# Kernel optimization log

Hardware: AMD Instinct MI355X
Metric: run time of the kernel (lower is better)

The kernel has to match this reference:

```python
import jax, jax.numpy as jnp
import numpy as np

EPS = 1e-5

def binary_activation(x):
    # ReActNet piecewise-polynomial STE: forward = sign(x), grad follows poly
    m1 = (x < -1).astype(x.dtype)
    m2 = (x < 0).astype(x.dtype)
    m3 = (x < 1).astype(x.dtype)
    out1 = -1.0 * m1 + (x * x + 2.0 * x) * (1.0 - m1)
    out2 = out1 * m2 + (-x * x + 2.0 * x) * (1.0 - m2)
    out3 = out2 * m3 + 1.0 * (1.0 - m3)
    return jax.lax.stop_gradient(jnp.sign(x) - out3) + out3

def binary_conv(x, w, stride, padding):
    # per-output-channel scaled sign weights with clamp STE
    scale = jnp.mean(jnp.abs(w), axis=(1, 2, 3), keepdims=True)
    clipped = jnp.clip(w, -1.0, 1.0)
    bw = jax.lax.stop_gradient(scale * jnp.sign(w) - clipped) + clipped
    return jax.lax.conv_general_dilated(
        x, bw, window_strides=(stride, stride),
        padding=[(padding, padding), (padding, padding)],
        dimension_numbers=('NCHW', 'OIHW', 'NCHW'))

def batch_norm(x, g, b):
    mu = jnp.mean(x, axis=(0, 2, 3), keepdims=True)
    var = jnp.mean((x - mu) ** 2, axis=(0, 2, 3), keepdims=True)
    xn = (x - mu) * jax.lax.rsqrt(var + EPS)
    return xn * g[None, :, None, None] + b[None, :, None, None]

def prelu(x, a):
    a = a[None, :, None, None]
    return jnp.where(x >= 0, x, a * x)

def setup_inputs() -> dict:
    key = jax.random.key(0)
    ks = jax.random.split(key, 12)
    N, C, H, W = 32, 256, 56, 56
    d = {
        'x': jax.random.normal(ks[0], (N, C, H, W), jnp.float32),
        'b11': jax.random.normal(ks[1], (1, C, 1, 1), jnp.float32) * 0.1,
        'b12': jax.random.normal(ks[2], (1, C, 1, 1), jnp.float32) * 0.1,
        'b13': jax.random.normal(ks[3], (1, C, 1, 1), jnp.float32) * 0.1,
        'b21': jax.random.normal(ks[4], (1, C, 1, 1), jnp.float32) * 0.1,
        'b22': jax.random.normal(ks[5], (1, C, 1, 1), jnp.float32) * 0.1,
        'b23': jax.random.normal(ks[6], (1, C, 1, 1), jnp.float32) * 0.1,
        'w3x3': jax.random.normal(ks[7], (C, C, 3, 3), jnp.float32) * 0.05,
        'wpw': jax.random.normal(ks[8], (C, C, 1, 1), jnp.float32) * 0.05,
        'g1': jnp.ones((C,), jnp.float32),
        'be1': jnp.zeros((C,), jnp.float32),
        'g2': jnp.ones((C,), jnp.float32),
        'be2': jnp.zeros((C,), jnp.float32),
        'p1': jnp.full((C,), 0.25, jnp.float32),
        'p2': jnp.full((C,), 0.25, jnp.float32),
    }
    return d

def reference(x, b11, b12, b13, b21, b22, b23, w3x3, wpw, g1, be1, g2, be2, p1, p2):
    # stride=1, inplanes == planes branch
    out1 = binary_activation(x + b11)
    out1 = binary_conv(out1, w3x3, stride=1, padding=1)
    out1 = batch_norm(out1, g1, be1)
    out1 = x + out1
    out1 = prelu(out1 + b12, p1) + b13
    out2 = binary_activation(out1 + b21)
    out2 = binary_conv(out2, wpw, stride=1, padding=0)
    out2 = batch_norm(out2, g2, be2)
    out2 = out2 + out1
    out2 = prelu(out2 + b22, p2) + b23
    return out2
```

## Files before the change

### kernel.cpp

```cpp
#include <hip/hip_runtime.h>

typedef __attribute__((ext_vector_type(4))) float  f32x4;
typedef __attribute__((ext_vector_type(4))) short  s16x4;
typedef __attribute__((ext_vector_type(4))) int    i32x4;

#define MFMAI8(a, b, c) __builtin_amdgcn_mfma_i32_16x16x64_i8((a), (b), (c), 0, 0, 0)

__device__ __forceinline__ void gload_lds16(const void* g, void* l) {
  __builtin_amdgcn_global_load_lds((const __attribute__((address_space(1))) void*)g,
                                   (__attribute__((address_space(3))) void*)l, 16, 0, 0);
}

__device__ __forceinline__ char sgn8(float v) {
  return v > 0.f ? (char)1 : (v < 0.f ? (char)-1 : (char)0);
}

__global__ __launch_bounds__(256) void prep_w(const float* __restrict__ w3,
                                              const float* __restrict__ wpw,
                                              char* __restrict__ w1s,
                                              char* __restrict__ w2s,
                                              float* __restrict__ scale1,
                                              float* __restrict__ scale2) {
  const int o = blockIdx.x;
  const int t = threadIdx.x;
  float s = 0.f;
  if (blockIdx.y == 0) {
    for (int u = t; u < 2304; u += 256) {
      int i = u / 9, tap = u % 9;
      float v = w3[(size_t)(o * 256 + i) * 9 + tap];
      s += fabsf(v);
      w1s[(size_t)(tap * 256 + o) * 256 + i] = sgn8(v);
    }
  } else {
    float v = wpw[o * 256 + t];
    s = fabsf(v);
    w2s[o * 256 + t] = sgn8(v);
  }
  for (int m = 1; m < 64; m <<= 1) s += __shfl_xor(s, m);
  __shared__ float red[4];
  if ((t & 63) == 0) red[t >> 6] = s;
  __syncthreads();
  if (t == 0) {
    float tot = red[0] + red[1] + red[2] + red[3];
    if (blockIdx.y == 0) scale1[o] = tot / 2304.f;
    else                 scale2[o] = tot / 256.f;
  }
}

__global__ __launch_bounds__(256) void sign_nhwc(const float* __restrict__ x,
                                                 const float* __restrict__ b11,
                                                 char* __restrict__ out) {
  __shared__ unsigned short l[56 * 128];
  __shared__ float cB[256];
  const int h = blockIdx.x, n = blockIdx.y, t = threadIdx.x;
  cB[t] = b11[t];
  __syncthreads();
  const int wv = t & 15, cg = t >> 4;
  if (wv < 14) {
    const int w0 = wv * 4;
    const int swz = (wv & 7) << 3;
#pragma unroll 4
    for (int it = 0; it < 8; ++it) {
      int cp = it * 16 + cg;
      int c0 = cp * 2;
      size_t i0 = (size_t)(n * 256 + c0) * 3136 + h * 56 + w0;
      f32x4 x0 = *(const f32x4*)(x + i0);
      f32x4 x1 = *(const f32x4*)(x + i0 + 3136);
      float bb0 = cB[c0], bb1 = cB[c0 + 1];
      int cs = cp ^ swz;
#pragma unroll
      for (int j = 0; j < 4; ++j) {
        unsigned short pk = (unsigned char)sgn8(x0[j] + bb0) |
                            ((unsigned short)(unsigned char)sgn8(x1[j] + bb1) << 8);
        l[(w0 + j) * 128 + cs] = pk;
      }
    }
  }
  __syncthreads();
  char* op = out + ((size_t)(n * 56 + h) * 56) * 256;
  for (int u = t; u < 56 * 16; u += 256) {
    int w2 = u >> 4, cp = u & 15;
    *(i32x4*)(op + w2 * 256 + cp * 16) =
        *(const i32x4*)&l[w2 * 128 + ((cp * 8) ^ (((w2 >> 2) & 7) << 3))];
  }
}

__global__ __launch_bounds__(256, 1) void conv3x3(const char* __restrict__ sIn,
                                                  const char* __restrict__ wSgn,
                                                  short* __restrict__ raw,
                                                  float* __restrict__ S,
                                                  float* __restrict__ SS) {
  __shared__ char lin[2][10 * 64 * 64];
  __shared__ char lw[2][9 * 64 * 64];

  int bid = (blockIdx.x & 7) * 112 + (blockIdx.x >> 3);
  const int ot = bid & 3;
  const int g  = bid >> 2;
  const int ht = g % 7, n = g / 7;
  const int h0 = ht * 8, oc0 = ot * 64;

  const int t = threadIdx.x;
  const int lane = t & 63, wv = t >> 6;
  const int cl = lane & 15, kk = lane >> 4;
  const int kswz = (kk ^ ((cl >> 1) & 3)) << 4;

  {
    i32x4* pl = (i32x4*)&lin[0][0];
    for (int u = t; u < 2 * 10 * 64 * 4; u += 256) pl[u] = (i32x4){0, 0, 0, 0};
  }
  __syncthreads();

  const int pw = t >> 2, sl = t & 3;
  const int srcslot = sl ^ (((1 + pw) >> 1) & 3);

#define STAGE_3x3(icc, bi)                                                          \
  {                                                                                 \
    if (t < 224) {                                                                  \
      _Pragma("unroll")                                                             \
      for (int rr = 0; rr < 10; ++rr) {                                             \
        int h = h0 - 1 + rr;                                                        \
        char* dst = &lin[bi][(rr * 64 + 1) * 64 + t * 16];                          \
        if (h >= 0 && h < 56) {                                                     \
          const char* src = sIn +                                                   \
              ((size_t)((n * 56 + h) * 56 + pw) * 256 + (icc) * 64 + srcslot * 16); \
          gload_lds16(src, dst);                                                    \
        } else {                                                                    \
          *(i32x4*)dst = (i32x4){0, 0, 0, 0};                                       \
        }                                                                           \
      }                                                                             \
    }                                                                               \
    _Pragma("unroll")                                                               \
    for (int i = 0; i < 9; ++i) {                                                   \
      int u = i * 256 + t;                                                          \
      int tap = u >> 8, oc_e = (u >> 2) & 63;                                       \
      int wslot = (u & 3) ^ ((u >> 3) & 3);                                         \
      const char* src = wSgn +                                                      \
          ((size_t)(tap * 256 + oc0 + oc_e) * 256 + (icc) * 64 + wslot * 16);       \
      gload_lds16(src, &lw[bi][u * 16]);                                            \
    }                                                                               \
  }

  int q0[7];
#pragma unroll
  for (int nf = 0; nf < 7; ++nf) {
    int p = wv * 112 + nf * 16 + cl;
    q0[nf] = (p / 56) * 64 + (p % 56);
  }

  i32x4 acc[4][7];
#pragma unroll
  for (int m = 0; m < 4; ++m)
#pragma unroll
    for (int nf = 0; nf < 7; ++nf) acc[m][nf] = (i32x4){0, 0, 0, 0};

  STAGE_3x3(0, 0);
  __syncthreads();

  for (int icc = 0; icc < 4; ++icc) {
    const int cur = icc & 1;
    if (icc < 3) STAGE_3x3(icc + 1, cur ^ 1);

#pragma unroll
    for (int kh = 0; kh < 3; ++kh)
#pragma unroll
      for (int kw = 0; kw < 3; ++kw) {
        const int tap = kh * 3 + kw;
        i32x4 a[4];
#pragma unroll
        for (int m = 0; m < 4; ++m)
          a[m] = *(const i32x4*)(&lw[cur][(tap * 64 + m * 16 + cl) * 64 + kswz]);
#pragma unroll
        for (int nf = 0; nf < 7; ++nf) {
          int qq = q0[nf] + kw;
          int addr = (qq + kh * 64) * 64 + ((kk ^ ((qq >> 1) & 3)) << 4);
          i32x4 b = *(const i32x4*)(&lin[cur][addr]);
#pragma unroll
          for (int m = 0; m < 4; ++m) acc[m][nf] = MFMAI8(a[m], b, acc[m][nf]);
        }
      }
    __syncthreads();
  }

#pragma unroll
  for (int m = 0; m < 4; ++m) {
    float sm[4] = {0.f, 0.f, 0.f, 0.f}, sq[4] = {0.f, 0.f, 0.f, 0.f};
#pragma unroll
    for (int nf = 0; nf < 7; ++nf) {
      int p = wv * 112 + nf * 16 + cl;
      int h = h0 + p / 56, w = p % 56;
      size_t base = ((size_t)n * 256 + oc0 + m * 16 + kk * 4) * 3136 + h * 56 + w;
      i32x4 v = acc[m][nf];
#pragma unroll
      for (int r2 = 0; r2 < 4; ++r2) {
        raw[base + (size_t)r2 * 3136] = (short)v[r2];
        float fv = (float)v[r2];
        sm[r2] += fv;
        sq[r2] += fv * fv;
      }
    }
#pragma unroll
    for (int r2 = 0; r2 < 4; ++r2) {
      float aa = sm[r2], qq = sq[r2];
      aa += __shfl_xor(aa, 1); qq += __shfl_xor(qq, 1);
      aa += __shfl_xor(aa, 2); qq += __shfl_xor(qq, 2);
      aa += __shfl_xor(aa, 4); qq += __shfl_xor(qq, 4);
      aa += __shfl_xor(aa, 8); qq += __shfl_xor(qq, 8);
      if (cl == 0) {
        int oc = oc0 + m * 16 + kk * 4 + r2;
        atomicAdd(&S[oc], aa);
        atomicAdd(&SS[oc], qq);
      }
    }
  }
}

__global__ __launch_bounds__(256, 2) void conv1x1(const char* __restrict__ sIn,
                                                  const char* __restrict__ wSgn,
                                                  short* __restrict__ raw,
                                                  float* __restrict__ S,
                                                  float* __restrict__ SS) {
  __shared__ char lin[2 * 112 * 64];
  __shared__ char lw[2 * 256 * 64];

  const int b = blockIdx.x;
  const int n = b / 28;
  const int hw0 = (b % 28) * 112;
  const size_t px0 = (size_t)n * 3136 + hw0;
  const int t = threadIdx.x, lane = t & 63, wv = t >> 6;
  const int cl = lane & 15, kk = lane >> 4;
  const int kswz = (kk ^ ((cl >> 1) & 3)) << 4;

#define STAGE_1x1(icc, bufi)                                                        \
  {                                                                                 \
    for (int u = t; u < 448; u += 256) {                                            \
      int srcslot = (u & 3) ^ ((u >> 3) & 3);                                       \
      const char* src = sIn + ((px0 + (u >> 2)) * 256 + (icc) * 64 + srcslot * 16); \
      gload_lds16(src, lin + (bufi) * 7168 + u * 16);                               \
    }                                                                               \
    _Pragma("unroll")                                                               \
    for (int i = 0; i < 4; ++i) {                                                   \
      int u = i * 256 + t;                                                          \
      int srcslot = (u & 3) ^ ((u >> 3) & 3);                                       \
      const char* src = wSgn + ((size_t)(u >> 2) * 256 + (icc) * 64 + srcslot * 16);\
      gload_lds16(src, lw + (bufi) * 16384 + u * 16);                               \
    }                                                                               \
  }

  i32x4 acc[4][7];
#pragma unroll
  for (int m = 0; m < 4; ++m)
#pragma unroll
    for (int nf = 0; nf < 7; ++nf) acc[m][nf] = (i32x4){0, 0, 0, 0};

  STAGE_1x1(0, 0);
  __syncthreads();
  for (int icc = 0; icc < 4; ++icc) {
    const int cur = icc & 1;
    if (icc < 3) STAGE_1x1(icc + 1, cur ^ 1);
    i32x4 bfr[7];
#pragma unroll
    for (int nf = 0; nf < 7; ++nf)
      bfr[nf] = *(const i32x4*)(lin + cur * 7168 + (nf * 16 + cl) * 64 + kswz);
#pragma unroll
    for (int m = 0; m < 4; ++m) {
      i32x4 a = *(const i32x4*)(lw + cur * 16384 + (wv * 64 + m * 16 + cl) * 64 + kswz);
#pragma unroll
      for (int nf = 0; nf < 7; ++nf) acc[m][nf] = MFMAI8(a, bfr[nf], acc[m][nf]);
    }
    __syncthreads();
  }

#pragma unroll
  for (int m = 0; m < 4; ++m) {
    float sm[4] = {0.f, 0.f, 0.f, 0.f}, sq[4] = {0.f, 0.f, 0.f, 0.f};
    size_t base0 = ((size_t)n * 256 + wv * 64 + m * 16 + kk * 4) * 3136 + hw0;
#pragma unroll
    for (int nf = 0; nf < 7; ++nf) {
      i32x4 v = acc[m][nf];
#pragma unroll
      for (int r2 = 0; r2 < 4; ++r2) {
        raw[base0 + (size_t)r2 * 3136 + nf * 16 + cl] = (short)v[r2];
        float fv = (float)v[r2];
        sm[r2] += fv;
        sq[r2] += fv * fv;
      }
    }
#pragma unroll
    for (int r2 = 0; r2 < 4; ++r2) {
      float aa = sm[r2], qq = sq[r2];
      aa += __shfl_xor(aa, 1); qq += __shfl_xor(qq, 1);
      aa += __shfl_xor(aa, 2); qq += __shfl_xor(qq, 2);
      aa += __shfl_xor(aa, 4); qq += __shfl_xor(qq, 4);
      aa += __shfl_xor(aa, 8); qq += __shfl_xor(qq, 8);
      if (cl == 0) {
        int oc = wv * 64 + m * 16 + kk * 4 + r2;
        atomicAdd(&S[oc], aa);
        atomicAdd(&SS[oc], qq);
      }
    }
  }
}

__global__ void bn_coef(const float* __restrict__ S, const float* __restrict__ SS,
                        const float* __restrict__ scale, const float* __restrict__ g,
                        const float* __restrict__ be, const float* __restrict__ bext,
                        float* __restrict__ A, float* __restrict__ B) {
  int o = threadIdx.x;
  const float invN = 1.f / 100352.f;
  float mu_r  = S[o] * invN;
  float var_r = SS[o] * invN - mu_r * mu_r;
  float sc    = scale[o];
  float rstd  = rsqrtf(sc * sc * var_r + 1e-5f);
  A[o] = g[o] * rstd * sc;
  B[o] = be[o] - g[o] * rstd * sc * mu_r + bext[o];
}

__global__ __launch_bounds__(256) void mid_fuse(const short* __restrict__ raw,
                                                const float* __restrict__ x,
                                                const float* __restrict__ A1,
                                                const float* __restrict__ B1,
                                                const float* __restrict__ p1,
                                                const float* __restrict__ b13,
                                                const float* __restrict__ b21,
                                                float* __restrict__ t1,
                                                char* __restrict__ s2) {
  __shared__ unsigned short l[56 * 128];
  __shared__ float cA[256], cB[256], cP[256], cD[256], cE[256];
  const int h = blockIdx.x, n = blockIdx.y, t = threadIdx.x;
  cA[t] = A1[t]; cB[t] = B1[t]; cP[t] = p1[t]; cD[t] = b13[t]; cE[t] = b21[t];
  __syncthreads();
  const int wv = t & 15, cg = t >> 4;
  if (wv < 14) {
    const int w0 = wv * 4;
    const int swz = (wv & 7) << 3;
#pragma unroll 2
    for (int it = 0; it < 8; ++it) {
      int cp = it * 16 + cg;
      int c0 = cp * 2;
      size_t i0 = (size_t)(n * 256 + c0) * 3136 + h * 56 + w0;
      f32x4 x0 = *(const f32x4*)(x + i0);
      f32x4 x1 = *(const f32x4*)(x + i0 + 3136);
      s16x4 r0 = *(const s16x4*)(raw + i0);
      s16x4 r1 = *(const s16x4*)(raw + i0 + 3136);
      float a0 = cA[c0], b0 = cB[c0], p0 = cP[c0], d0 = cD[c0], e0 = cE[c0];
      float a1 = cA[c0+1], b1 = cB[c0+1], p1v = cP[c0+1], d1 = cD[c0+1], e1 = cE[c0+1];
      f32x4 o0, o1;
      int cs = cp ^ swz;
#pragma unroll
      for (int j = 0; j < 4; ++j) {
        float u0 = x0[j] + a0 * (float)r0[j] + b0;
        u0 = (u0 >= 0.f ? u0 : p0 * u0) + d0;
        o0[j] = u0;
        float u1 = x1[j] + a1 * (float)r1[j] + b1;
        u1 = (u1 >= 0.f ? u1 : p1v * u1) + d1;
        o1[j] = u1;
        unsigned short pk = (unsigned char)sgn8(u0 + e0) |
                            ((unsigned short)(unsigned char)sgn8(u1 + e1) << 8);
        l[(w0 + j) * 128 + cs] = pk;
      }
      *(f32x4*)(t1 + i0) = o0;
      *(f32x4*)(t1 + i0 + 3136) = o1;
    }
  }
  __syncthreads();
  char* op = s2 + ((size_t)(n * 56 + h) * 56) * 256;
  for (int u = t; u < 56 * 16; u += 256) {
    int w2 = u >> 4, cp = u & 15;
    *(i32x4*)(op + w2 * 256 + cp * 16) =
        *(const i32x4*)&l[w2 * 128 + ((cp * 8) ^ (((w2 >> 2) & 7) << 3))];
  }
}

__global__ __launch_bounds__(256) void final_fuse(const short* __restrict__ raw,
                                                  const float* __restrict__ A2,
                                                  const float* __restrict__ B2,
                                                  const float* __restrict__ p2,
                                                  const float* __restrict__ b23,
                                                  float* out) {
  const int c = blockIdx.x & 255;
  const size_t base = (size_t)blockIdx.x * 3136;
  const float a = A2[c], b = B2[c], p = p2[c], d = b23[c];
  for (int i = threadIdx.x; i < 784; i += 256) {
    s16x4 r  = *(const s16x4*)(raw + base + (size_t)i * 4);
    f32x4 tt = *(const f32x4*)(out + base + (size_t)i * 4);
    f32x4 o;
#pragma unroll
    for (int j = 0; j < 4; ++j) {
      float v = a * (float)r[j] + b + tt[j];
      o[j] = (v >= 0.f ? v : p * v) + d;
    }
    *(f32x4*)(out + base + (size_t)i * 4) = o;
  }
}

extern "C" void kernel_launch(void* const* d_in, const int* in_sizes, int n_in,
                              void* d_out, int out_size, void* d_ws, size_t ws_size,
                              hipStream_t stream) {
  const float* x   = (const float*)d_in[0];
  const float* b11 = (const float*)d_in[1];
  const float* b12 = (const float*)d_in[2];
  const float* b13 = (const float*)d_in[3];
  const float* b21 = (const float*)d_in[4];
  const float* b22 = (const float*)d_in[5];
  const float* b23 = (const float*)d_in[6];
  const float* w3  = (const float*)d_in[7];
  const float* wpw = (const float*)d_in[8];
  const float* g1  = (const float*)d_in[9];
  const float* be1 = (const float*)d_in[10];
  const float* g2  = (const float*)d_in[11];
  const float* be2 = (const float*)d_in[12];
  const float* p1  = (const float*)d_in[13];
  const float* p2  = (const float*)d_in[14];

  char* ws = (char*)d_ws;
  short* raw    = (short*)(ws);
  char*  sgn    = (char*)(ws + 51380224);
  char*  w1s    = (char*)(ws + 77070336);
  char*  w2s    = (char*)(ws + 77660160);
  float* scale1 = (float*)(ws + 77725696);
  float* scale2 = (float*)(ws + 77726720);
  float* S1     = (float*)(ws + 77727744);
  float* SS1    = (float*)(ws + 77728768);
  float* S2     = (float*)(ws + 77729792);
  float* SS2    = (float*)(ws + 77730816);
  float* A1     = (float*)(ws + 77731840);
  float* B1     = (float*)(ws + 77732864);
  float* A2     = (float*)(ws + 77733888);
  float* B2     = (float*)(ws + 77734912);
  float* t1     = (float*)d_out;

  hipMemsetAsync(ws + 77727744, 0, 4096, stream);

  prep_w<<<dim3(256, 2), 256, 0, stream>>>(w3, wpw, w1s, w2s, scale1, scale2);
  sign_nhwc<<<dim3(56, 32), 256, 0, stream>>>(x, b11, sgn);
  conv3x3<<<dim3(896), 256, 0, stream>>>(sgn, w1s, raw, S1, SS1);
  bn_coef<<<1, 256, 0, stream>>>(S1, SS1, scale1, g1, be1, b12, A1, B1);
  mid_fuse<<<dim3(56, 32), 256, 0, stream>>>(raw, x, A1, B1, p1, b13, b21, t1, sgn);
  conv1x1<<<dim3(896), 256, 0, stream>>>(sgn, w2s, raw, S2, SS2);
  bn_coef<<<1, 256, 0, stream>>>(S2, SS2, scale2, g2, be2, b22, A2, B2);
  final_fuse<<<dim3(8192), 256, 0, stream>>>(raw, A2, B2, p2, b23, (float*)d_out);
}
```

Baseline: 393.1 us.

## Read conv weights directly from global memory and shrink LDS staging

New measurement: 416.1 us. 1.06x slower.

```diff
diff --git a/kernel.cpp b/kernel.cpp
--- a/kernel.cpp
+++ b/kernel.cpp
@@ -85,13 +85,12 @@
   }
 }
 
-__global__ __launch_bounds__(256, 1) void conv3x3(const char* __restrict__ sIn,
+__global__ __launch_bounds__(256, 2) void conv3x3(const char* __restrict__ sIn,
                                                   const char* __restrict__ wSgn,
                                                   short* __restrict__ raw,
                                                   float* __restrict__ S,
                                                   float* __restrict__ SS) {
-  __shared__ char lin[2][10 * 64 * 64];
-  __shared__ char lw[2][9 * 64 * 64];
+  __shared__ char lin[2][10 * 58 * 64];
 
   int bid = (blockIdx.x & 7) * 112 + (blockIdx.x >> 3);
   const int ot = bid & 3;
@@ -102,11 +101,10 @@
   const int t = threadIdx.x;
   const int lane = t & 63, wv = t >> 6;
   const int cl = lane & 15, kk = lane >> 4;
-  const int kswz = (kk ^ ((cl >> 1) & 3)) << 4;
 
   {
     i32x4* pl = (i32x4*)&lin[0][0];
-    for (int u = t; u < 2 * 10 * 64 * 4; u += 256) pl[u] = (i32x4){0, 0, 0, 0};
+    for (int u = t; u < 2 * 10 * 58 * 4; u += 256) pl[u] = (i32x4){0, 0, 0, 0};
   }
   __syncthreads();
 
@@ -119,7 +117,7 @@
       _Pragma("unroll")                                                             \
       for (int rr = 0; rr < 10; ++rr) {                                             \
         int h = h0 - 1 + rr;                                                        \
-        char* dst = &lin[bi][(rr * 64 + 1) * 64 + t * 16];                          \
+        char* dst = &lin[bi][(rr * 58 + 1 + pw) * 64 + sl * 16];                    \
         if (h >= 0 && h < 56) {                                                     \
           const char* src = sIn +                                                   \
               ((size_t)((n * 56 + h) * 56 + pw) * 256 + (icc) * 64 + srcslot * 16); \
@@ -129,22 +127,14 @@
         }                                                                           \
       }                                                                             \
     }                                                                               \
-    _Pragma("unroll")                                                               \
-    for (int i = 0; i < 9; ++i) {                                                   \
-      int u = i * 256 + t;                                                          \
-      int tap = u >> 8, oc_e = (u >> 2) & 63;                                       \
-      int wslot = (u & 3) ^ ((u >> 3) & 3);                                         \
-      const char* src = wSgn +                                                      \
-          ((size_t)(tap * 256 + oc0 + oc_e) * 256 + (icc) * 64 + wslot * 16);       \
-      gload_lds16(src, &lw[bi][u * 16]);                                            \
-    }                                                                               \
-  }
-
-  int q0[7];
+  }
+
+  int r0[7], c0[7];
 #pragma unroll
   for (int nf = 0; nf < 7; ++nf) {
     int p = wv * 112 + nf * 16 + cl;
-    q0[nf] = (p / 56) * 64 + (p % 56);
+    r0[nf] = p / 56;
+    c0[nf] = p % 56;
   }
 
   i32x4 acc[4][7];
@@ -168,11 +158,12 @@
         i32x4 a[4];
 #pragma unroll
         for (int m = 0; m < 4; ++m)
-          a[m] = *(const i32x4*)(&lw[cur][(tap * 64 + m * 16 + cl) * 64 + kswz]);
+          a[m] = *(const i32x4*)(wSgn +
+              (((size_t)(tap * 256 + oc0 + m * 16 + cl)) << 8) + icc * 64 + kk * 16);
 #pragma unroll
         for (int nf = 0; nf < 7; ++nf) {
-          int qq = q0[nf] + kw;
-          int addr = (qq + kh * 64) * 64 + ((kk ^ ((qq >> 1) & 3)) << 4);
+          int col = c0[nf] + kw;
+          int addr = ((r0[nf] + kh) * 58 + col) * 64 + ((kk ^ ((col >> 1) & 3)) << 4);
           i32x4 b = *(const i32x4*)(&lin[cur][addr]);
 #pragma unroll
           for (int m = 0; m < 4; ++m) acc[m][nf] = MFMAI8(a[m], b, acc[m][nf]);
@@ -219,8 +210,7 @@
                                                   short* __restrict__ raw,
                                                   float* __restrict__ S,
                                                   float* __restrict__ SS) {
-  __shared__ char lin[2 * 112 * 64];
-  __shared__ char lw[2 * 256 * 64];
+  __shared__ char lin[112 * 256];
 
   const int b = blockIdx.x;
   const int n = b / 28;
@@ -228,22 +218,13 @@
   const size_t px0 = (size_t)n * 3136 + hw0;
   const int t = threadIdx.x, lane = t & 63, wv = t >> 6;
   const int cl = lane & 15, kk = lane >> 4;
-  const int kswz = (kk ^ ((cl >> 1) & 3)) << 4;
-
-#define STAGE_1x1(icc, bufi)                                                        \
-  {                                                                                 \
-    for (int u = t; u < 448; u += 256) {                                            \
-      int srcslot = (u & 3) ^ ((u >> 3) & 3);                                       \
-      const char* src = sIn + ((px0 + (u >> 2)) * 256 + (icc) * 64 + srcslot * 16); \
-      gload_lds16(src, lin + (bufi) * 7168 + u * 16);                               \
-    }                                                                               \
-    _Pragma("unroll")                                                               \
-    for (int i = 0; i < 4; ++i) {                                                   \
-      int u = i * 256 + t;                                                          \
-      int srcslot = (u & 3) ^ ((u >> 3) & 3);                                       \
-      const char* src = wSgn + ((size_t)(u >> 2) * 256 + (icc) * 64 + srcslot * 16);\
-      gload_lds16(src, lw + (bufi) * 16384 + u * 16);                               \
-    }                                                                               \
+
+#pragma unroll
+  for (int i = 0; i < 7; ++i) {
+    int u = i * 256 + t;
+    int px = u >> 4, s = u & 15;
+    const char* src = sIn + (px0 + px) * 256 + ((s ^ (px & 7)) * 16);
+    gload_lds16(src, lin + u * 16);
   }
 
   i32x4 acc[4][7];
@@ -252,22 +233,24 @@
 #pragma unroll
     for (int nf = 0; nf < 7; ++nf) acc[m][nf] = (i32x4){0, 0, 0, 0};
 
-  STAGE_1x1(0, 0);
-  __syncthreads();
+  __syncthreads();
+
+#pragma unroll
   for (int icc = 0; icc < 4; ++icc) {
-    const int cur = icc & 1;
-    if (icc < 3) STAGE_1x1(icc + 1, cur ^ 1);
     i32x4 bfr[7];
 #pragma unroll
-    for (int nf = 0; nf < 7; ++nf)
-      bfr[nf] = *(const i32x4*)(lin + cur * 7168 + (nf * 16 + cl) * 64 + kswz);
+    for (int nf = 0; nf < 7; ++nf) {
+      int px = nf * 16 + cl;
+      int srd = (icc * 4 + kk) ^ (px & 7);
+      bfr[nf] = *(const i32x4*)(lin + px * 256 + srd * 16);
+    }
 #pragma unroll
     for (int m = 0; m < 4; ++m) {
-      i32x4 a = *(const i32x4*)(lw + cur * 16384 + (wv * 64 + m * 16 + cl) * 64 + kswz);
+      i32x4 a = *(const i32x4*)(wSgn +
+          (((size_t)(wv * 64 + m * 16 + cl)) << 8) + icc * 64 + kk * 16);
 #pragma unroll
       for (int nf = 0; nf < 7; ++nf) acc[m][nf] = MFMAI8(a, bfr[nf], acc[m][nf]);
     }
-    __syncthreads();
   }
 
 #pragma unroll
```
